# Kernel tuning notes

Hardware: AMD Instinct MI355X
Metric: run time of the kernel (lower is better)

The kernel has to match this reference:

```python
import jax, jax.numpy as jnp
import numpy as np

NUM_JOINTS = 21
WINDOW = 131072  # window_size; pose3d has WINDOW+1 frames
N_BONES = NUM_JOINTS - 1
W_PROJ, W_BONE, W_SMOOTH, W_LIFT = 1.0, 1.0, 0.5, 0.1


def setup_inputs() -> dict:
    key = jax.random.key(0)
    k1, k2, k3, k4, k5 = jax.random.split(key, 5)
    pose3d = jax.random.normal(k1, (WINDOW + 1, 3, NUM_JOINTS), dtype=jnp.float32)
    camera_proj = jax.random.normal(k2, (WINDOW, 2, 3), dtype=jnp.float32)
    pose_2d = jax.random.normal(k3, (WINDOW, 2, NUM_JOINTS), dtype=jnp.float32)
    bone_lengths = jax.random.uniform(k4, (N_BONES,), dtype=jnp.float32)
    lift_directions = jax.random.normal(k5, (WINDOW, 3, N_BONES), dtype=jnp.float32)
    # normalize lift directions to unit vectors (they are bone directions)
    lift_directions = lift_directions / jnp.linalg.norm(lift_directions, axis=1, keepdims=True)
    # kinematic-chain bone connections: (child, parent) = (i+1, i), guaranteed distinct
    child = jnp.arange(1, NUM_JOINTS, dtype=jnp.int32)
    parent = jnp.arange(0, NUM_JOINTS - 1, dtype=jnp.int32)
    bone_connections = jnp.stack([child, parent], axis=1)  # [N_BONES, 2]
    lift_bone_connections = bone_connections
    return {
        "pose3d": pose3d,
        "camera_proj": camera_proj,
        "pose_2d": pose_2d,
        "bone_lengths": bone_lengths,
        "lift_directions": lift_directions,
        "bone_connections": bone_connections,
        "lift_bone_connections": lift_bone_connections,
    }


def reference(pose3d, camera_proj, pose_2d, bone_lengths, lift_directions,
              bone_connections, lift_bone_connections):
    J = NUM_JOINTS
    # --- projection loss: per-frame 2x3 camera applied to frames 1: ---
    projected = jnp.einsum('wij,wjk->wik', camera_proj, pose3d[1:])  # [W,2,J]
    proj_loss = jnp.sum(jnp.square(projected - pose_2d)) / (2 * J)
    # --- bone length loss ---
    d = pose3d[:, :, bone_connections[:, 0]] - pose3d[:, :, bone_connections[:, 1]]  # [W+1,3,NB]
    length_of_bone = jnp.sum(jnp.square(d), axis=1)  # [W+1, NB]
    bone_loss = jnp.sum(jnp.square(length_of_bone - bone_lengths[None, :])) / (J - 1)
    # --- smoothness loss (second difference) ---
    vel = pose3d[1:] - pose3d[:-1]  # [W,3,J]
    smooth_loss = jnp.sum(jnp.square(vel[1:] - vel[:-1])) / (3 * J)
    # --- lift direction loss ---
    bv = pose3d[1:, :, lift_bone_connections[:, 0]] - pose3d[1:, :, lift_bone_connections[:, 1]]  # [W,3,NB]
    norm = jnp.linalg.norm(bv, axis=1, keepdims=True)  # [W,1,NB]
    est_dirs = bv / norm
    lift_loss = jnp.sum(jnp.square(lift_directions - est_dirs)) / (3 * J)
    return (W_PROJ * proj_loss + W_BONE * bone_loss
            + W_SMOOTH * smooth_loss + W_LIFT * lift_loss)
```

## Files before the change

### kernel.cpp

```cpp
#include <hip/hip_runtime.h>
#include <math.h>

#define W 131072
#define FR 63
#define NB 20
#define FPB 32
#define BLKT 128
#define TFR (FPB + 2)
#define SP_PAD 2144
#define NBLOCKS (W / FPB)

__global__ __launch_bounds__(BLKT) void loss_pass1(
    const float* __restrict__ pose3d,
    const float* __restrict__ cam,
    const float* __restrict__ p2d,
    const float* __restrict__ blen,
    const float* __restrict__ ldir,
    const int* __restrict__ bcon,
    const int* __restrict__ lcon,
    float* __restrict__ partial)
{
  __shared__ float sP[SP_PAD];
  __shared__ float sWave[2];

  const int tid = threadIdx.x;
  const int blk = blockIdx.x;
  const int f0 = blk * FPB;
  const int s  = tid & 3;
  const int fl = tid >> 2;
  const int w  = f0 + fl;

  {
    const float* src = pose3d + (size_t)f0 * FR;
    const int avail = ((W + 1) - f0) * FR;
#pragma unroll
    for (int it = 0; it < 5; ++it) {
      int q = tid + it * BLKT;
      if (q < SP_PAD / 4) {
        int j = 4 * q;
        if (j + 4 <= avail) {
          *(float4*)(sP + j) = *(const float4*)(src + j);
        } else {
#pragma unroll
          for (int k = 0; k < 4; ++k)
            sP[j + k] = (j + k < avail) ? src[j + k] : 0.0f;
        }
      }
    }
  }
  __syncthreads();

  const float* P0 = sP + fl * FR;
  const float* P1 = P0 + FR;
  const float* P2 = P1 + FR;

  float acc_smooth = 0.0f;
  if (w < W - 1) {
#pragma unroll
    for (int k = 0; k < 16; ++k) {
      int e = 16 * s + k;
      if (e < FR) {
        float d2 = P2[e] - 2.0f * P1[e] + P0[e];
        acc_smooth += d2 * d2;
      }
    }
  }

  float acc_proj = 0.0f;
  {
    const float2* cp = (const float2*)(cam + (size_t)w * 6);
    float2 ca = cp[0], cb = cp[1], cc = cp[2];
    const float* pr = p2d + (size_t)w * 42;
#pragma unroll
    for (int k = 0; k < 6; ++k) {
      int j = s + 4 * k;
      if (j < 21) {
        float x = P1[j], y = P1[21 + j], z = P1[42 + j];
        float p0 = ca.x * x + ca.y * y + cb.x * z;
        float p1v = cb.y * x + cc.x * y + cc.y * z;
        float d0 = p0 - pr[j];
        float d1 = p1v - pr[21 + j];
        acc_proj += d0 * d0 + d1 * d1;
      }
    }
  }

  float acc_bone = 0.0f, acc_lift = 0.0f;
  {
    const int2* bc2 = (const int2*)bcon;
    const int2* lc2 = (const int2*)lcon;
    const float* lr = ldir + (size_t)w * 60;
#pragma unroll
    for (int k = 0; k < 5; ++k) {
      int b = s + 4 * k;
      int2 lc = lc2[b];
      float dx = P1[lc.x]      - P1[lc.y];
      float dy = P1[21 + lc.x] - P1[21 + lc.y];
      float dz = P1[42 + lc.x] - P1[42 + lc.y];
      float S = dx * dx + dy * dy + dz * dz;
      float inv = rsqrtf(S);
      float ex = lr[b]      - dx * inv;
      float ey = lr[20 + b] - dy * inv;
      float ez = lr[40 + b] - dz * inv;
      acc_lift += ex * ex + ey * ey + ez * ez;

      int2 bc = bc2[b];
      float Sb = S;
      if (bc.x != lc.x || bc.y != lc.y) {
        float bx = P1[bc.x]      - P1[bc.y];
        float by = P1[21 + bc.x] - P1[21 + bc.y];
        float bz = P1[42 + bc.x] - P1[42 + bc.y];
        Sb = bx * bx + by * by + bz * bz;
      }
      float t = Sb - blen[b];
      acc_bone += t * t;
    }
    if (w == 0) {
#pragma unroll
      for (int k = 0; k < 5; ++k) {
        int b = s + 4 * k;
        int2 bc = bc2[b];
        float bx = P0[bc.x]      - P0[bc.y];
        float by = P0[21 + bc.x] - P0[21 + bc.y];
        float bz = P0[42 + bc.x] - P0[42 + bc.y];
        float Sb = bx * bx + by * by + bz * bz;
        float t = Sb - blen[b];
        acc_bone += t * t;
      }
    }
  }

  float tot = acc_proj * (1.0f / 42.0f) + acc_bone * (1.0f / 20.0f)
            + acc_smooth * (0.5f / 63.0f) + acc_lift * (0.1f / 63.0f);
#pragma unroll
  for (int off = 32; off > 0; off >>= 1) tot += __shfl_xor(tot, off, 64);
  if ((tid & 63) == 0) sWave[tid >> 6] = tot;
  __syncthreads();
  if (tid == 0) partial[blk] = sWave[0] + sWave[1];
}

__global__ __launch_bounds__(256) void loss_pass2(
    const float* __restrict__ partial, float* __restrict__ out)
{
  __shared__ float sW[4];
  int tid = threadIdx.x;
  float s = 0.0f;
#pragma unroll
  for (int i = 0; i < NBLOCKS / 256; ++i) s += partial[i * 256 + tid];
#pragma unroll
  for (int off = 32; off > 0; off >>= 1) s += __shfl_xor(s, off, 64);
  if ((tid & 63) == 0) sW[tid >> 6] = s;
  __syncthreads();
  if (tid == 0) {
    float t = 0.0f;
#pragma unroll
    for (int i = 0; i < 4; ++i) t += sW[i];
    out[0] = t;
  }
}

extern "C" void kernel_launch(void* const* d_in, const int* in_sizes, int n_in,
                              void* d_out, int out_size, void* d_ws, size_t ws_size,
                              hipStream_t stream) {
  const float* pose3d = (const float*)d_in[0];
  const float* cam    = (const float*)d_in[1];
  const float* p2d    = (const float*)d_in[2];
  const float* blen   = (const float*)d_in[3];
  const float* ldir   = (const float*)d_in[4];
  const int*   bcon   = (const int*)d_in[5];
  const int*   lcon   = (const int*)d_in[6];
  float* out     = (float*)d_out;
  float* partial = (float*)d_ws;

  loss_pass1<<<NBLOCKS, BLKT, 0, stream>>>(pose3d, cam, p2d, blen, ldir,
                                           bcon, lcon, partial);
  loss_pass2<<<1, 256, 0, stream>>>(partial, out);
}
```

Baseline: 126.1 us.

## Compute smoothness from global float4 loads and add chain-bone fast path

Moves the second-difference smoothness term to direct vectorized global loads, overlapped with shared-memory staging before the barrier. Trims the staging buffer and drops the tail guards. Adds a runtime-checked fast path for consecutive-chain bone connections that loads each joint once into registers. The unaligned float4 global loads and the slight over-read at the last block are risks.

Result: slower. 130.3 us (+3.3%).

```diff
diff --git a/kernel.cpp b/kernel.cpp
--- a/kernel.cpp
+++ b/kernel.cpp
@@ -3,12 +3,11 @@
 
 #define W 131072
 #define FR 63
-#define NB 20
 #define FPB 32
 #define BLKT 128
-#define TFR (FPB + 2)
-#define SP_PAD 2144
 #define NBLOCKS (W / FPB)
+#define STG4 520
+#define SMOOTH_TOT ((W - 1) * FR)
 
 __global__ __launch_bounds__(BLKT) void loss_pass1(
     const float* __restrict__ pose3d,
@@ -20,66 +19,71 @@
     const int* __restrict__ lcon,
     float* __restrict__ partial)
 {
-  __shared__ float sP[SP_PAD];
+  __shared__ float sP[STG4 * 4];
   __shared__ float sWave[2];
 
   const int tid = threadIdx.x;
   const int blk = blockIdx.x;
   const int f0 = blk * FPB;
+  const float* src = pose3d + (size_t)f0 * FR;
+
+  {
+    float4* s4 = (float4*)sP;
+    const float4* g4 = (const float4*)src;
+#pragma unroll
+    for (int it = 0; it < 5; ++it) {
+      int q = tid + it * BLKT;
+      if (q < STG4) s4[q] = g4[q];
+    }
+  }
+
+  float acc_smooth = 0.0f;
+  {
+    const int lim = (blk == NBLOCKS - 1) ? (SMOOTH_TOT - f0 * FR) : (FPB * FR);
+#pragma unroll
+    for (int g = 0; g < 4; ++g) {
+      int o = tid * 16 + 4 * g;
+      if (o + 4 <= lim) {
+        float4 A = *(const float4*)(src + o);
+        float4 B = *(const float4*)(src + o + 63);
+        float4 C = *(const float4*)(src + o + 126);
+        float dx = C.x - 2.0f * B.x + A.x;
+        float dy = C.y - 2.0f * B.y + A.y;
+        float dz = C.z - 2.0f * B.z + A.z;
+        float dw = C.w - 2.0f * B.w + A.w;
+        acc_smooth += dx * dx + dy * dy + dz * dz + dw * dw;
+      } else {
+#pragma unroll
+        for (int e = 0; e < 4; ++e) {
+          int oo = o + e;
+          if (oo < lim) {
+            float d2 = src[oo + 126] - 2.0f * src[oo + 63] + src[oo];
+            acc_smooth += d2 * d2;
+          }
+        }
+      }
+    }
+  }
+  __syncthreads();
+
   const int s  = tid & 3;
   const int fl = tid >> 2;
   const int w  = f0 + fl;
-
-  {
-    const float* src = pose3d + (size_t)f0 * FR;
-    const int avail = ((W + 1) - f0) * FR;
-#pragma unroll
-    for (int it = 0; it < 5; ++it) {
-      int q = tid + it * BLKT;
-      if (q < SP_PAD / 4) {
-        int j = 4 * q;
-        if (j + 4 <= avail) {
-          *(float4*)(sP + j) = *(const float4*)(src + j);
-        } else {
-#pragma unroll
-          for (int k = 0; k < 4; ++k)
-            sP[j + k] = (j + k < avail) ? src[j + k] : 0.0f;
-        }
-      }
-    }
-  }
-  __syncthreads();
-
-  const float* P0 = sP + fl * FR;
-  const float* P1 = P0 + FR;
-  const float* P2 = P1 + FR;
-
-  float acc_smooth = 0.0f;
-  if (w < W - 1) {
-#pragma unroll
-    for (int k = 0; k < 16; ++k) {
-      int e = 16 * s + k;
-      if (e < FR) {
-        float d2 = P2[e] - 2.0f * P1[e] + P0[e];
-        acc_smooth += d2 * d2;
-      }
-    }
-  }
+  const float* P1 = sP + (fl + 1) * FR;
 
   float acc_proj = 0.0f;
   {
-    const float2* cp = (const float2*)(cam + (size_t)w * 6);
-    float2 ca = cp[0], cb = cp[1], cc = cp[2];
+    const float* cp = cam + (size_t)w * 6;
+    float c00 = cp[0], c01 = cp[1], c02 = cp[2];
+    float c10 = cp[3], c11 = cp[4], c12 = cp[5];
     const float* pr = p2d + (size_t)w * 42;
 #pragma unroll
     for (int k = 0; k < 6; ++k) {
       int j = s + 4 * k;
       if (j < 21) {
         float x = P1[j], y = P1[21 + j], z = P1[42 + j];
-        float p0 = ca.x * x + ca.y * y + cb.x * z;
-        float p1v = cb.y * x + cc.x * y + cc.y * z;
-        float d0 = p0 - pr[j];
-        float d1 = p1v - pr[21 + j];
+        float d0 = c00 * x + c01 * y + c02 * z - pr[j];
+        float d1 = c10 * x + c11 * y + c12 * z - pr[21 + j];
         acc_proj += d0 * d0 + d1 * d1;
       }
     }
@@ -90,41 +94,77 @@
     const int2* bc2 = (const int2*)bcon;
     const int2* lc2 = (const int2*)lcon;
     const float* lr = ldir + (size_t)w * 60;
+    float bl[5], lx[5], ly[5], lz[5];
+    bool ch = true;
 #pragma unroll
     for (int k = 0; k < 5; ++k) {
-      int b = s + 4 * k;
+      int b = 5 * s + k;
       int2 lc = lc2[b];
-      float dx = P1[lc.x]      - P1[lc.y];
-      float dy = P1[21 + lc.x] - P1[21 + lc.y];
-      float dz = P1[42 + lc.x] - P1[42 + lc.y];
-      float S = dx * dx + dy * dy + dz * dz;
-      float inv = rsqrtf(S);
-      float ex = lr[b]      - dx * inv;
-      float ey = lr[20 + b] - dy * inv;
-      float ez = lr[40 + b] - dz * inv;
-      acc_lift += ex * ex + ey * ey + ez * ez;
-
       int2 bc = bc2[b];
-      float Sb = S;
-      if (bc.x != lc.x || bc.y != lc.y) {
-        float bx = P1[bc.x]      - P1[bc.y];
-        float by = P1[21 + bc.x] - P1[21 + bc.y];
-        float bz = P1[42 + bc.x] - P1[42 + bc.y];
-        Sb = bx * bx + by * by + bz * bz;
-      }
-      float t = Sb - blen[b];
-      acc_bone += t * t;
+      ch = ch && (lc.x == b + 1) && (lc.y == b) && (bc.x == b + 1) && (bc.y == b);
+      bl[k] = blen[b];
+      lx[k] = lr[b];
+      ly[k] = lr[20 + b];
+      lz[k] = lr[40 + b];
+    }
+    if (__all(ch)) {
+      float Jx[6], Jy[6], Jz[6];
+#pragma unroll
+      for (int m = 0; m < 6; ++m) {
+        int j = 5 * s + m;
+        Jx[m] = P1[j]; Jy[m] = P1[21 + j]; Jz[m] = P1[42 + j];
+      }
+#pragma unroll
+      for (int k = 0; k < 5; ++k) {
+        float dx = Jx[k + 1] - Jx[k];
+        float dy = Jy[k + 1] - Jy[k];
+        float dz = Jz[k + 1] - Jz[k];
+        float S = dx * dx + dy * dy + dz * dz;
+        float inv = rsqrtf(S);
+        float ex = lx[k] - dx * inv;
+        float ey = ly[k] - dy * inv;
+        float ez = lz[k] - dz * inv;
+        acc_lift += ex * ex + ey * ey + ez * ez;
+        float t = S - bl[k];
+        acc_bone += t * t;
+      }
+    } else {
+#pragma unroll
+      for (int k = 0; k < 5; ++k) {
+        int b = 5 * s + k;
+        int2 lc = lc2[b];
+        float dx = P1[lc.x]      - P1[lc.y];
+        float dy = P1[21 + lc.x] - P1[21 + lc.y];
+        float dz = P1[42 + lc.x] - P1[42 + lc.y];
+        float S = dx * dx + dy * dy + dz * dz;
+        float inv = rsqrtf(S);
+        float ex = lx[k] - dx * inv;
+        float ey = ly[k] - dy * inv;
+        float ez = lz[k] - dz * inv;
+        acc_lift += ex * ex + ey * ey + ez * ez;
+        int2 bc = bc2[b];
+        float Sb = S;
+        if (bc.x != lc.x || bc.y != lc.y) {
+          float bx = P1[bc.x]      - P1[bc.y];
+          float by = P1[21 + bc.x] - P1[21 + bc.y];
+          float bz = P1[42 + bc.x] - P1[42 + bc.y];
+          Sb = bx * bx + by * by + bz * bz;
+        }
+        float t = Sb - bl[k];
+        acc_bone += t * t;
+      }
     }
     if (w == 0) {
+      const float* P0 = sP;
 #pragma unroll
       for (int k = 0; k < 5; ++k) {
-        int b = s + 4 * k;
+        int b = 5 * s + k;
         int2 bc = bc2[b];
         float bx = P0[bc.x]      - P0[bc.y];
         float by = P0[21 + bc.x] - P0[21 + bc.y];
         float bz = P0[42 + bc.x] - P0[42 + bc.y];
         float Sb = bx * bx + by * by + bz * bz;
-        float t = Sb - blen[b];
+        float t = Sb - bl[k];
         acc_bone += t * t;
       }
     }
```

## Stage all per-frame inputs in LDS with coalesced float4 loads, halve frames per block

Applied to the files above, without the earlier changes.

Each block now copies its slices of pose_2d, lift directions, camera matrices and the bone tables into shared memory with coalesced float4 loads, instead of having each thread make strided per-frame global reads. Frames per block drop from 32 to 16 with 8 threads per frame, and the smoothness term is computed over a flat element index across the block. This targets uncoalesced global access, at the cost of more shared memory per block, twice as many blocks, and a larger second-pass reduction.

New measurement: 131.6 us. +4.4%, slower.

```diff
diff --git a/kernel.cpp b/kernel.cpp
--- a/kernel.cpp
+++ b/kernel.cpp
@@ -3,12 +3,15 @@
 
 #define W 131072
 #define FR 63
-#define NB 20
-#define FPB 32
+#define FPB 16
 #define BLKT 128
-#define TFR (FPB + 2)
-#define SP_PAD 2144
 #define NBLOCKS (W / FPB)
+#define POSE_F 1134
+#define POSE_Q 284
+#define P2D_Q 168
+#define LDIR_Q 240
+#define CAM_Q 24
+#define SMOOTH_TOT ((W - 1) * FR)
 
 __global__ __launch_bounds__(BLKT) void loss_pass1(
     const float* __restrict__ pose3d,
@@ -20,66 +23,100 @@
     const int* __restrict__ lcon,
     float* __restrict__ partial)
 {
-  __shared__ float sP[SP_PAD];
+  __shared__ float sPose[POSE_Q * 4];
+  __shared__ float sP2d[P2D_Q * 4];
+  __shared__ float sLdir[LDIR_Q * 4];
+  __shared__ float sCam[CAM_Q * 4];
+  __shared__ int   sBC[40], sLC[40];
+  __shared__ float sBlen[20];
   __shared__ float sWave[2];
 
   const int tid = threadIdx.x;
   const int blk = blockIdx.x;
   const int f0 = blk * FPB;
-  const int s  = tid & 3;
-  const int fl = tid >> 2;
+
+  {
+    const float4* g = (const float4*)(pose3d + (size_t)f0 * FR);
+    float4* d = (float4*)sPose;
+    const int avail = ((W + 1) - f0) * FR;
+#pragma unroll
+    for (int it = 0; it < 3; ++it) {
+      int q = tid + it * BLKT;
+      if (q < POSE_Q) {
+        int j = 4 * q;
+        if (j + 4 <= avail) d[q] = g[q];
+        else {
+          const float* gs = (const float*)g;
+#pragma unroll
+          for (int k = 0; k < 4; ++k)
+            sPose[j + k] = (j + k < avail) ? gs[j + k] : 0.0f;
+        }
+      }
+    }
+  }
+  {
+    const float4* g = (const float4*)(p2d + (size_t)f0 * 42);
+    float4* d = (float4*)sP2d;
+#pragma unroll
+    for (int it = 0; it < 2; ++it) {
+      int q = tid + it * BLKT;
+      if (q < P2D_Q) d[q] = g[q];
+    }
+  }
+  {
+    const float4* g = (const float4*)(ldir + (size_t)f0 * 60);
+    float4* d = (float4*)sLdir;
+#pragma unroll
+    for (int it = 0; it < 2; ++it) {
+      int q = tid + it * BLKT;
+      if (q < LDIR_Q) d[q] = g[q];
+    }
+  }
+  {
+    const float4* g = (const float4*)(cam + (size_t)f0 * 6);
+    float4* d = (float4*)sCam;
+    if (tid < CAM_Q) d[tid] = g[tid];
+  }
+  if (tid < 40) { sBC[tid] = bcon[tid]; sLC[tid] = lcon[tid]; }
+  else if (tid < 60) sBlen[tid - 40] = blen[tid - 40];
+  __syncthreads();
+
+  float acc_smooth = 0.0f;
+  {
+    const int n_s_all = FPB * FR;
+    const int n_s = (blk == NBLOCKS - 1) ? (SMOOTH_TOT - f0 * FR) : n_s_all;
+#pragma unroll
+    for (int c = 0; c < 2; ++c) {
+      int o = c * 512 + 4 * tid;
+#pragma unroll
+      for (int e = 0; e < 4; ++e) {
+        int oo = o + e;
+        if (oo < n_s) {
+          float d2 = sPose[oo + 126] - 2.0f * sPose[oo + 63] + sPose[oo];
+          acc_smooth += d2 * d2;
+        }
+      }
+    }
+  }
+
+  const int s  = tid & 7;
+  const int fl = tid >> 3;
   const int w  = f0 + fl;
-
-  {
-    const float* src = pose3d + (size_t)f0 * FR;
-    const int avail = ((W + 1) - f0) * FR;
-#pragma unroll
-    for (int it = 0; it < 5; ++it) {
-      int q = tid + it * BLKT;
-      if (q < SP_PAD / 4) {
-        int j = 4 * q;
-        if (j + 4 <= avail) {
-          *(float4*)(sP + j) = *(const float4*)(src + j);
-        } else {
-#pragma unroll
-          for (int k = 0; k < 4; ++k)
-            sP[j + k] = (j + k < avail) ? src[j + k] : 0.0f;
-        }
-      }
-    }
-  }
-  __syncthreads();
-
-  const float* P0 = sP + fl * FR;
-  const float* P1 = P0 + FR;
-  const float* P2 = P1 + FR;
-
-  float acc_smooth = 0.0f;
-  if (w < W - 1) {
-#pragma unroll
-    for (int k = 0; k < 16; ++k) {
-      int e = 16 * s + k;
-      if (e < FR) {
-        float d2 = P2[e] - 2.0f * P1[e] + P0[e];
-        acc_smooth += d2 * d2;
-      }
-    }
-  }
+  const float* P1 = sPose + (fl + 1) * FR;
 
   float acc_proj = 0.0f;
   {
-    const float2* cp = (const float2*)(cam + (size_t)w * 6);
-    float2 ca = cp[0], cb = cp[1], cc = cp[2];
-    const float* pr = p2d + (size_t)w * 42;
-#pragma unroll
-    for (int k = 0; k < 6; ++k) {
-      int j = s + 4 * k;
+    const float* cp = sCam + fl * 6;
+    float c00 = cp[0], c01 = cp[1], c02 = cp[2];
+    float c10 = cp[3], c11 = cp[4], c12 = cp[5];
+    const float* pr = sP2d + fl * 42;
+#pragma unroll
+    for (int k = 0; k < 3; ++k) {
+      int j = s + 8 * k;
       if (j < 21) {
         float x = P1[j], y = P1[21 + j], z = P1[42 + j];
-        float p0 = ca.x * x + ca.y * y + cb.x * z;
-        float p1v = cb.y * x + cc.x * y + cc.y * z;
-        float d0 = p0 - pr[j];
-        float d1 = p1v - pr[21 + j];
+        float d0 = c00 * x + c01 * y + c02 * z - pr[j];
+        float d1 = c10 * x + c11 * y + c12 * z - pr[21 + j];
         acc_proj += d0 * d0 + d1 * d1;
       }
     }
@@ -87,45 +124,48 @@
 
   float acc_bone = 0.0f, acc_lift = 0.0f;
   {
-    const int2* bc2 = (const int2*)bcon;
-    const int2* lc2 = (const int2*)lcon;
-    const float* lr = ldir + (size_t)w * 60;
-#pragma unroll
-    for (int k = 0; k < 5; ++k) {
-      int b = s + 4 * k;
-      int2 lc = lc2[b];
-      float dx = P1[lc.x]      - P1[lc.y];
-      float dy = P1[21 + lc.x] - P1[21 + lc.y];
-      float dz = P1[42 + lc.x] - P1[42 + lc.y];
-      float S = dx * dx + dy * dy + dz * dz;
-      float inv = rsqrtf(S);
-      float ex = lr[b]      - dx * inv;
-      float ey = lr[20 + b] - dy * inv;
-      float ez = lr[40 + b] - dz * inv;
-      acc_lift += ex * ex + ey * ey + ez * ez;
-
-      int2 bc = bc2[b];
-      float Sb = S;
-      if (bc.x != lc.x || bc.y != lc.y) {
-        float bx = P1[bc.x]      - P1[bc.y];
-        float by = P1[21 + bc.x] - P1[21 + bc.y];
-        float bz = P1[42 + bc.x] - P1[42 + bc.y];
-        Sb = bx * bx + by * by + bz * bz;
-      }
-      float t = Sb - blen[b];
-      acc_bone += t * t;
-    }
-    if (w == 0) {
-#pragma unroll
-      for (int k = 0; k < 5; ++k) {
-        int b = s + 4 * k;
-        int2 bc = bc2[b];
-        float bx = P0[bc.x]      - P0[bc.y];
-        float by = P0[21 + bc.x] - P0[21 + bc.y];
-        float bz = P0[42 + bc.x] - P0[42 + bc.y];
-        float Sb = bx * bx + by * by + bz * bz;
-        float t = Sb - blen[b];
+    const float* lr = sLdir + fl * 60;
+#pragma unroll
+    for (int k = 0; k < 3; ++k) {
+      int b = s + 8 * k;
+      if (b < 20) {
+        int lcx = sLC[2 * b], lcy = sLC[2 * b + 1];
+        float dx = P1[lcx]      - P1[lcy];
+        float dy = P1[21 + lcx] - P1[21 + lcy];
+        float dz = P1[42 + lcx] - P1[42 + lcy];
+        float S = dx * dx + dy * dy + dz * dz;
+        float inv = rsqrtf(S);
+        float ex = lr[b]      - dx * inv;
+        float ey = lr[20 + b] - dy * inv;
+        float ez = lr[40 + b] - dz * inv;
+        acc_lift += ex * ex + ey * ey + ez * ez;
+
+        int bcx = sBC[2 * b], bcy = sBC[2 * b + 1];
+        float Sb = S;
+        if (bcx != lcx || bcy != lcy) {
+          float bx = P1[bcx]      - P1[bcy];
+          float by = P1[21 + bcx] - P1[21 + bcy];
+          float bz = P1[42 + bcx] - P1[42 + bcy];
+          Sb = bx * bx + by * by + bz * bz;
+        }
+        float t = Sb - sBlen[b];
         acc_bone += t * t;
+      }
+    }
+    if (w == 0 && fl == 0) {
+      const float* P0 = sPose;
+#pragma unroll
+      for (int k = 0; k < 3; ++k) {
+        int b = s + 8 * k;
+        if (b < 20) {
+          int bcx = sBC[2 * b], bcy = sBC[2 * b + 1];
+          float bx = P0[bcx]      - P0[bcy];
+          float by = P0[21 + bcx] - P0[21 + bcy];
+          float bz = P0[42 + bcx] - P0[42 + bcy];
+          float Sb = bx * bx + by * by + bz * bz;
+          float t = Sb - sBlen[b];
+          acc_bone += t * t;
+        }
       }
     }
   }
```

## Remap threads to flat element indexing and read pose directly from global memory

Applied to the files above, without the earlier changes.

Drops the shared-memory staging of the pose window. Each loss term is now computed over flattened per-block work items: one element per thread for smoothness, one (frame, joint) pair for projection, and one (frame, bone) pair for bone and lift. Camera, connection and bone-length data go into shared memory, and the block size doubles to 256 with an occupancy hint. Coalescing for the smoothness reads should improve, but pose reads now go through L1/L2 with redundant and uncoalesced gathers, and the integer divisions add cost.

Measured after the change: 128.0 us. About the same (+1.5%).

```diff
diff --git a/kernel.cpp b/kernel.cpp
--- a/kernel.cpp
+++ b/kernel.cpp
@@ -3,14 +3,12 @@
 
 #define W 131072
 #define FR 63
-#define NB 20
 #define FPB 32
-#define BLKT 128
-#define TFR (FPB + 2)
-#define SP_PAD 2144
+#define BLKT 256
 #define NBLOCKS (W / FPB)
+#define SMOOTH_TOT ((W - 1) * FR)
 
-__global__ __launch_bounds__(BLKT) void loss_pass1(
+__global__ __launch_bounds__(BLKT, 8) void loss_pass1(
     const float* __restrict__ pose3d,
     const float* __restrict__ cam,
     const float* __restrict__ p2d,
@@ -20,112 +18,90 @@
     const int* __restrict__ lcon,
     float* __restrict__ partial)
 {
-  __shared__ float sP[SP_PAD];
-  __shared__ float sWave[2];
+  __shared__ float sCam[FPB * 6];
+  __shared__ float sBlen[20];
+  __shared__ int   sBC[40], sLC[40];
+  __shared__ float sWave[4];
 
   const int tid = threadIdx.x;
   const int blk = blockIdx.x;
   const int f0 = blk * FPB;
-  const int s  = tid & 3;
-  const int fl = tid >> 2;
-  const int w  = f0 + fl;
+  const float* src = pose3d + (size_t)f0 * FR;
 
   {
-    const float* src = pose3d + (size_t)f0 * FR;
-    const int avail = ((W + 1) - f0) * FR;
-#pragma unroll
-    for (int it = 0; it < 5; ++it) {
-      int q = tid + it * BLKT;
-      if (q < SP_PAD / 4) {
-        int j = 4 * q;
-        if (j + 4 <= avail) {
-          *(float4*)(sP + j) = *(const float4*)(src + j);
-        } else {
-#pragma unroll
-          for (int k = 0; k < 4; ++k)
-            sP[j + k] = (j + k < avail) ? src[j + k] : 0.0f;
-        }
-      }
-    }
+    if (tid < 48) ((float4*)sCam)[tid] = ((const float4*)(cam + (size_t)f0 * 6))[tid];
+    if (tid >= 64 && tid < 104) { int i = tid - 64; sBC[i] = bcon[i]; sLC[i] = lcon[i]; }
+    if (tid >= 128 && tid < 148) sBlen[tid - 128] = blen[tid - 128];
   }
   __syncthreads();
 
-  const float* P0 = sP + fl * FR;
-  const float* P1 = P0 + FR;
-  const float* P2 = P1 + FR;
+  float acc_smooth = 0.0f, acc_proj = 0.0f, acc_bone = 0.0f, acc_lift = 0.0f;
 
-  float acc_smooth = 0.0f;
-  if (w < W - 1) {
+  {
+    const int lim = (blk == NBLOCKS - 1) ? (SMOOTH_TOT - f0 * FR) : (FPB * FR);
 #pragma unroll
-    for (int k = 0; k < 16; ++k) {
-      int e = 16 * s + k;
-      if (e < FR) {
-        float d2 = P2[e] - 2.0f * P1[e] + P0[e];
+    for (int k = 0; k < 8; ++k) {
+      int o = k * BLKT + tid;
+      if (o < lim) {
+        float d2 = src[o + 126] - 2.0f * src[o + 63] + src[o];
         acc_smooth += d2 * d2;
       }
     }
   }
 
-  float acc_proj = 0.0f;
-  {
-    const float2* cp = (const float2*)(cam + (size_t)w * 6);
-    float2 ca = cp[0], cb = cp[1], cc = cp[2];
-    const float* pr = p2d + (size_t)w * 42;
 #pragma unroll
-    for (int k = 0; k < 6; ++k) {
-      int j = s + 4 * k;
-      if (j < 21) {
-        float x = P1[j], y = P1[21 + j], z = P1[42 + j];
-        float p0 = ca.x * x + ca.y * y + cb.x * z;
-        float p1v = cb.y * x + cc.x * y + cc.y * z;
-        float d0 = p0 - pr[j];
-        float d1 = p1v - pr[21 + j];
-        acc_proj += d0 * d0 + d1 * d1;
-      }
+  for (int k = 0; k < 3; ++k) {
+    int t = k * BLKT + tid;
+    if (t < FPB * 21) {
+      int f = t / 21;
+      int j = t - 21 * f;
+      const float* P1 = src + (f + 1) * FR;
+      float x = P1[j], y = P1[21 + j], z = P1[42 + j];
+      const float* cp = sCam + 6 * f;
+      const float* pr = p2d + (size_t)(f0 + f) * 42;
+      float d0 = cp[0] * x + cp[1] * y + cp[2] * z - pr[j];
+      float d1 = cp[3] * x + cp[4] * y + cp[5] * z - pr[21 + j];
+      acc_proj += d0 * d0 + d1 * d1;
     }
   }
 
-  float acc_bone = 0.0f, acc_lift = 0.0f;
-  {
-    const int2* bc2 = (const int2*)bcon;
-    const int2* lc2 = (const int2*)lcon;
-    const float* lr = ldir + (size_t)w * 60;
 #pragma unroll
-    for (int k = 0; k < 5; ++k) {
-      int b = s + 4 * k;
-      int2 lc = lc2[b];
-      float dx = P1[lc.x]      - P1[lc.y];
-      float dy = P1[21 + lc.x] - P1[21 + lc.y];
-      float dz = P1[42 + lc.x] - P1[42 + lc.y];
+  for (int k = 0; k < 3; ++k) {
+    int t = k * BLKT + tid;
+    if (t < FPB * 20) {
+      int f = t / 20;
+      int b = t - 20 * f;
+      const float* P1 = src + (f + 1) * FR;
+      int lcx = sLC[2 * b], lcy = sLC[2 * b + 1];
+      float dx = P1[lcx]      - P1[lcy];
+      float dy = P1[21 + lcx] - P1[21 + lcy];
+      float dz = P1[42 + lcx] - P1[42 + lcy];
       float S = dx * dx + dy * dy + dz * dz;
       float inv = rsqrtf(S);
+      const float* lr = ldir + (size_t)(f0 + f) * 60;
       float ex = lr[b]      - dx * inv;
       float ey = lr[20 + b] - dy * inv;
       float ez = lr[40 + b] - dz * inv;
       acc_lift += ex * ex + ey * ey + ez * ez;
 
-      int2 bc = bc2[b];
+      int bcx = sBC[2 * b], bcy = sBC[2 * b + 1];
       float Sb = S;
-      if (bc.x != lc.x || bc.y != lc.y) {
-        float bx = P1[bc.x]      - P1[bc.y];
-        float by = P1[21 + bc.x] - P1[21 + bc.y];
-        float bz = P1[42 + bc.x] - P1[42 + bc.y];
+      if (bcx != lcx || bcy != lcy) {
+        float bx = P1[bcx]      - P1[bcy];
+        float by = P1[21 + bcx] - P1[21 + bcy];
+        float bz = P1[42 + bcx] - P1[42 + bcy];
         Sb = bx * bx + by * by + bz * bz;
       }
-      float t = Sb - blen[b];
-      acc_bone += t * t;
-    }
-    if (w == 0) {
-#pragma unroll
-      for (int k = 0; k < 5; ++k) {
-        int b = s + 4 * k;
-        int2 bc = bc2[b];
-        float bx = P0[bc.x]      - P0[bc.y];
-        float by = P0[21 + bc.x] - P0[21 + bc.y];
-        float bz = P0[42 + bc.x] - P0[42 + bc.y];
-        float Sb = bx * bx + by * by + bz * bz;
-        float t = Sb - blen[b];
-        acc_bone += t * t;
+      float tt = Sb - sBlen[b];
+      acc_bone += tt * tt;
+
+      if (blk == 0 && t < 20) {
+        float bx = src[bcx]      - src[bcy];
+        float by = src[21 + bcx] - src[21 + bcy];
+        float bz = src[42 + bcx] - src[42 + bcy];
+        float S0 = bx * bx + by * by + bz * bz;
+        float t0 = S0 - sBlen[b];
+        acc_bone += t0 * t0;
       }
     }
   }
@@ -136,7 +112,7 @@
   for (int off = 32; off > 0; off >>= 1) tot += __shfl_xor(tot, off, 64);
   if ((tid & 63) == 0) sWave[tid >> 6] = tot;
   __syncthreads();
-  if (tid == 0) partial[blk] = sWave[0] + sWave[1];
+  if (tid == 0) partial[blk] = (sWave[0] + sWave[1]) + (sWave[2] + sWave[3]);
 }
 
 __global__ __launch_bounds__(256) void loss_pass2(
```
